# Kernel optimization log

Hardware: AMD Instinct MI355X
Metric: run time of the kernel (lower is better)

Reference implementation:

```python
import jax, jax.numpy as jnp
import numpy as np

E, D, H = 8, 512, 2048  # num_experts, features, features*mlp_ratio
B, S = 4, 512


def _lecun(key, shape):
    fan_in = shape[-2] if len(shape) >= 2 else shape[0]
    return jax.random.normal(key, shape, dtype=jnp.float32) / jnp.sqrt(jnp.float32(fan_in))


def setup_inputs() -> dict:
    key = jax.random.key(0)
    ks = jax.random.split(key, 8)
    return {
        'x_real': jax.random.normal(ks[0], (B, S, D), dtype=jnp.float32),
        'x_imag': jax.random.normal(ks[1], (B, S, D), dtype=jnp.float32),
        # gating Dense over concat([amp, phase]) -> in_features = 2*D
        'gate_W': _lecun(ks[2], (2 * D, E)),
        'gate_b': jnp.zeros((E,), jnp.float32),
        # per-expert ComplexLinear 1: D -> H
        'W1r': _lecun(ks[3], (E, D, H)),
        'W1i': _lecun(ks[4], (E, D, H)),
        'b1r': jnp.zeros((E, H), jnp.float32),
        'b1i': jnp.zeros((E, H), jnp.float32),
        # per-expert ComplexModReLU bias
        'mod_b': jnp.zeros((E, H), jnp.float32),
        # per-expert ComplexLinear 2: H -> D
        'W2r': _lecun(ks[5], (E, H, D)),
        'W2i': _lecun(ks[6], (E, H, D)),
        'b2r': jnp.zeros((E, D), jnp.float32),
        'b2i': jnp.zeros((E, D), jnp.float32),
    }


def reference(x_real, x_imag, gate_W, gate_b, W1r, W1i, b1r, b1i, mod_b, W2r, W2i, b2r, b2i):
    eps = 1e-10
    # --- gating: scores over [|z|, angle(z)] ---
    amp = jnp.sqrt(x_real ** 2 + x_imag ** 2)            # |z|, [B,S,D]
    phase = jnp.arctan2(x_imag, x_real)                  # angle(z)
    routing_input = jnp.concatenate([amp, phase], axis=-1)  # [B,S,2D]
    scores = routing_input @ gate_W + gate_b             # [B,S,E]
    probs = jax.nn.softmax(scores, axis=-1)
    idx = jnp.argmax(probs, axis=-1)                     # [B,S] top-1 expert

    # --- all experts dense (faithful to reference): complex linear 1 ---
    # (Wr + iWi)(xr + ixi) : hr = xr Wr - xi Wi ; hi = xr Wi + xi Wr
    h_r = (jnp.einsum('bsd,edh->ebsh', x_real, W1r)
           - jnp.einsum('bsd,edh->ebsh', x_imag, W1i)) + b1r[:, None, None, :]
    h_i = (jnp.einsum('bsd,edh->ebsh', x_real, W1i)
           + jnp.einsum('bsd,edh->ebsh', x_imag, W1r)) + b1i[:, None, None, :]

    # --- ComplexModReLU: relu(|z|+b) * z / (|z|+eps), |z| = sqrt(r^2+i^2+eps) ---
    a = jnp.sqrt(h_r ** 2 + h_i ** 2 + eps)              # [E,B,S,H]
    scale = jax.nn.relu(a + mod_b[:, None, None, :]) / (a + eps)
    h_r = h_r * scale
    h_i = h_i * scale

    # --- complex linear 2 ---
    o_r = (jnp.einsum('ebsh,ehd->ebsd', h_r, W2r)
           - jnp.einsum('ebsh,ehd->ebsd', h_i, W2i)) + b2r[:, None, None, :]
    o_i = (jnp.einsum('ebsh,ehd->ebsd', h_r, W2i)
           + jnp.einsum('ebsh,ehd->ebsd', h_i, W2r)) + b2i[:, None, None, :]

    # --- mask + weight (top-1): out = sum_e out_e * probs[...,e] * (argmax==e) ---
    e_ids = jnp.arange(probs.shape[-1])
    w = jnp.transpose(probs, (2, 0, 1)) * (idx[None, :, :] == e_ids[:, None, None])  # [E,B,S]
    out_r = jnp.einsum('ebs,ebsd->bsd', w, o_r)
    out_i = jnp.einsum('ebs,ebsd->bsd', w, o_i)
    return (out_r, out_i)
```

## Files before the change

kernel.cpp:

```cpp
#include <hip/hip_runtime.h>
#include <math.h>

#define NE 8
#define ND 512
#define NH 2048
#define NT 2048

typedef __attribute__((ext_vector_type(8))) short short8;
typedef __attribute__((ext_vector_type(4))) float f32x4;

#define GLL(g, d) __builtin_amdgcn_global_load_lds( \
    (const __attribute__((address_space(1))) void*)(g), \
    (__attribute__((address_space(3))) void*)(d), 16, 0, 0)

__device__ __forceinline__ unsigned short f2bf(float x) {
    unsigned int u = __builtin_bit_cast(unsigned int, x);
    u += 0x7FFFu + ((u >> 16) & 1u);
    return (unsigned short)(u >> 16);
}

__device__ __forceinline__ short8 neg8(short8 v) {
    int4 u = __builtin_bit_cast(int4, v);
    u.x ^= 0x80008000; u.y ^= 0x80008000; u.z ^= 0x80008000; u.w ^= 0x80008000;
    return __builtin_bit_cast(short8, u);
}

__device__ __forceinline__ short8 lds8(const unsigned short* p) {
    return *(const short8*)p;
}

__global__ __launch_bounds__(256) void gate_kernel(
    const float* __restrict__ xr, const float* __restrict__ xi,
    const float* __restrict__ gW, const float* __restrict__ gb,
    float* __restrict__ gate_w,
    int* __restrict__ counts, int* __restrict__ tok_list)
{
    int t = blockIdx.x;
    int tid = threadIdx.x;
    const float* xrt = xr + (size_t)t * ND;
    const float* xit = xi + (size_t)t * ND;

    float acc[NE] = {0,0,0,0,0,0,0,0};
    for (int r = tid; r < 2 * ND; r += 256) {
        int d = r & (ND - 1);
        float a = xrt[d], b = xit[d];
        float v = (r < ND) ? sqrtf(a * a + b * b) : atan2f(b, a);
        const float4* g = (const float4*)(gW + (size_t)r * NE);
        float4 g0 = g[0], g1 = g[1];
        acc[0] += v * g0.x; acc[1] += v * g0.y; acc[2] += v * g0.z; acc[3] += v * g0.w;
        acc[4] += v * g1.x; acc[5] += v * g1.y; acc[6] += v * g1.z; acc[7] += v * g1.w;
    }
    #pragma unroll
    for (int e = 0; e < NE; e++) {
        for (int off = 32; off > 0; off >>= 1)
            acc[e] += __shfl_down(acc[e], off, 64);
    }
    __shared__ float part[4][NE];
    int wave = tid >> 6, lane = tid & 63;
    if (lane == 0) {
        #pragma unroll
        for (int e = 0; e < NE; e++) part[wave][e] = acc[e];
    }
    __syncthreads();
    if (tid == 0) {
        float s[NE];
        #pragma unroll
        for (int e = 0; e < NE; e++)
            s[e] = part[0][e] + part[1][e] + part[2][e] + part[3][e] + gb[e];
        int amax = 0; float m = s[0];
        #pragma unroll
        for (int e = 1; e < NE; e++) if (s[e] > m) { m = s[e]; amax = e; }
        float denom = 0.f;
        #pragma unroll
        for (int e = 0; e < NE; e++) denom += expf(s[e] - m);
        gate_w[t] = 1.0f / denom;
        int pos = atomicAdd(&counts[amax], 1);
        tok_list[amax * NT + pos] = t;
    }
}

__global__ __launch_bounds__(256) void convx_kernel(
    const float* __restrict__ xr, const float* __restrict__ xi,
    unsigned short* __restrict__ obr, unsigned short* __restrict__ obi)
{
    int i = blockIdx.x * 256 + threadIdx.x;
    float4 vr = ((const float4*)xr)[i];
    float4 vi = ((const float4*)xi)[i];
    ((ushort4*)obr)[i] = make_ushort4(f2bf(vr.x), f2bf(vr.y), f2bf(vr.z), f2bf(vr.w));
    ((ushort4*)obi)[i] = make_ushort4(f2bf(vi.x), f2bf(vi.y), f2bf(vi.z), f2bf(vi.w));
}

__global__ __launch_bounds__(256) void transw_kernel(
    const float* __restrict__ s0, unsigned short* __restrict__ d0,
    const float* __restrict__ s1, unsigned short* __restrict__ d1,
    int R, int C)
{
    __shared__ float tile[64][65];
    int e = blockIdx.z;
    int c0 = blockIdx.x * 64, r0 = blockIdx.y * 64;
    size_t off = (size_t)e * R * C;
    int tid = threadIdx.x;
    #pragma unroll
    for (int p = 0; p < 2; ++p) {
        const float* src = (p ? s1 : s0) + off;
        unsigned short* dst = (p ? d1 : d0) + off;
        if (p) __syncthreads();
        for (int i = 0; i < 16; ++i) {
            int idx = tid + i * 256;
            int r = idx >> 6, c = idx & 63;
            tile[r][c] = src[(size_t)(r0 + r) * C + c0 + c];
        }
        __syncthreads();
        for (int i = 0; i < 16; ++i) {
            int idx = tid + i * 256;
            int c = idx >> 6, r = idx & 63;
            dst[(size_t)(c0 + c) * R + r0 + r] = f2bf(tile[r][c]);
        }
    }
}

__global__ __launch_bounds__(256, 4) void moe1_kernel(
    const unsigned short* __restrict__ xbr, const unsigned short* __restrict__ xbi,
    const unsigned short* __restrict__ w1tr, const unsigned short* __restrict__ w1ti,
    const float* __restrict__ b1r, const float* __restrict__ b1i,
    const float* __restrict__ mod_b,
    const int* __restrict__ counts, const int* __restrict__ tok_list,
    unsigned short* __restrict__ hr, unsigned short* __restrict__ hi)
{
    int e = blockIdx.z;
    int n = counts[e];
    int mbase = blockIdx.y * 64;
    if (mbase >= n) return;
    int n0 = blockIdx.x * 64;
    int tid = threadIdx.x;
    int w = tid >> 6, l = tid & 63;
    int l15 = l & 15, quad = l >> 4;

    __shared__ unsigned short sAr[64 * 64];
    __shared__ unsigned short sAi[64 * 64];
    __shared__ unsigned short sBr[64 * 64];
    __shared__ unsigned short sBi[64 * 64];
    __shared__ int toks[64];

    const int* tl = tok_list + e * NT;
    if (tid < 64) {
        int idx = mbase + tid;
        toks[tid] = tl[idx < n ? idx : n - 1];
    }
    __syncthreads();

    int swz = (((l & 7) ^ ((l >> 3) & 7)) * 8);
    int ra0 = toks[w * 16 + (l >> 3)];
    int ra1 = toks[w * 16 + 8 + (l >> 3)];
    const unsigned short* gAr0 = xbr + (size_t)ra0 * ND + swz;
    const unsigned short* gAi0 = xbi + (size_t)ra0 * ND + swz;
    const unsigned short* gAr1 = xbr + (size_t)ra1 * ND + swz;
    const unsigned short* gAi1 = xbi + (size_t)ra1 * ND + swz;
    size_t brow = (size_t)e * NH + n0 + w * 16 + (l >> 3);
    const unsigned short* gBr0 = w1tr + brow * ND + swz;
    const unsigned short* gBr1 = w1tr + (brow + 8) * ND + swz;
    const unsigned short* gBi0 = w1ti + brow * ND + swz;
    const unsigned short* gBi1 = w1ti + (brow + 8) * ND + swz;

    unsigned short* dAr0 = sAr + (w * 16) * 64;
    unsigned short* dAr1 = sAr + (w * 16 + 8) * 64;
    unsigned short* dAi0 = sAi + (w * 16) * 64;
    unsigned short* dAi1 = sAi + (w * 16 + 8) * 64;
    unsigned short* dBr0 = sBr + (w * 16) * 64;
    unsigned short* dBr1 = sBr + (w * 16 + 8) * 64;
    unsigned short* dBi0 = sBi + (w * 16) * 64;
    unsigned short* dBi1 = sBi + (w * 16 + 8) * 64;

    f32x4 accr[4] = {}, acci[4] = {};

    for (int kt = 0; kt < ND / 64; ++kt) {
        __syncthreads();
        int ko = kt * 64;
        GLL(gAr0 + ko, dAr0); GLL(gAi0 + ko, dAi0);
        GLL(gAr1 + ko, dAr1); GLL(gAi1 + ko, dAi1);
        GLL(gBr0 + ko, dBr0); GLL(gBr1 + ko, dBr1);
        GLL(gBi0 + ko, dBi0); GLL(gBi1 + ko, dBi1);
        __syncthreads();
        #pragma unroll
        for (int ks = 0; ks < 2; ++ks) {
            int pa = ((ks * 4 + quad) ^ (l15 & 7)) * 8;
            short8 br  = lds8(sBr + (w * 16 + l15) * 64 + pa);
            short8 bi2 = lds8(sBi + (w * 16 + l15) * 64 + pa);
            #pragma unroll
            for (int m = 0; m < 4; ++m) {
                short8 ar  = lds8(sAr + (m * 16 + l15) * 64 + pa);
                short8 ai2 = lds8(sAi + (m * 16 + l15) * 64 + pa);
                short8 an  = neg8(ai2);
                accr[m] = __builtin_amdgcn_mfma_f32_16x16x32_bf16(ar,  br,  accr[m], 0, 0, 0);
                accr[m] = __builtin_amdgcn_mfma_f32_16x16x32_bf16(an,  bi2, accr[m], 0, 0, 0);
                acci[m] = __builtin_amdgcn_mfma_f32_16x16x32_bf16(ar,  bi2, acci[m], 0, 0, 0);
                acci[m] = __builtin_amdgcn_mfma_f32_16x16x32_bf16(ai2, br,  acci[m], 0, 0, 0);
            }
        }
    }

    int col = n0 + w * 16 + l15;
    float bre = b1r[(size_t)e * NH + col];
    float bie = b1i[(size_t)e * NH + col];
    float mbv = mod_b[(size_t)e * NH + col];
    #pragma unroll
    for (int m = 0; m < 4; ++m) {
        #pragma unroll
        for (int r = 0; r < 4; ++r) {
            int tix = m * 16 + quad * 4 + r;
            if (mbase + tix >= n) continue;
            int tok = toks[tix];
            float vr = accr[m][r] + bre;
            float vi = acci[m][r] + bie;
            float a = sqrtf(vr * vr + vi * vi + 1e-10f);
            float sc = fmaxf(a + mbv, 0.0f) / (a + 1e-10f);
            hr[(size_t)tok * NH + col] = f2bf(vr * sc);
            hi[(size_t)tok * NH + col] = f2bf(vi * sc);
        }
    }
}

__global__ __launch_bounds__(256, 4) void moe2_kernel(
    const unsigned short* __restrict__ hr, const unsigned short* __restrict__ hi,
    const unsigned short* __restrict__ w2tr, const unsigned short* __restrict__ w2ti,
    const float* __restrict__ b2r, const float* __restrict__ b2i,
    const int* __restrict__ counts, const int* __restrict__ tok_list,
    const float* __restrict__ gate_w,
    float* __restrict__ out)
{
    int e = blockIdx.z >> 2;
    int ksl = blockIdx.z & 3;
    int n = counts[e];
    int mbase = blockIdx.y * 64;
    if (mbase >= n) return;
    int n0 = blockIdx.x * 64;
    int kbase = ksl * (NH / 4);
    int tid = threadIdx.x;
    int w = tid >> 6, l = tid & 63;
    int l15 = l & 15, quad = l >> 4;

    __shared__ unsigned short sAr[64 * 64];
    __shared__ unsigned short sAi[64 * 64];
    __shared__ unsigned short sBr[64 * 64];
    __shared__ unsigned short sBi[64 * 64];
    __shared__ int toks[64];

    const int* tl = tok_list + e * NT;
    if (tid < 64) {
        int idx = mbase + tid;
        toks[tid] = tl[idx < n ? idx : n - 1];
    }
    __syncthreads();

    int swz = (((l & 7) ^ ((l >> 3) & 7)) * 8);
    int ra0 = toks[w * 16 + (l >> 3)];
    int ra1 = toks[w * 16 + 8 + (l >> 3)];
    const unsigned short* gAr0 = hr + (size_t)ra0 * NH + kbase + swz;
    const unsigned short* gAi0 = hi + (size_t)ra0 * NH + kbase + swz;
    const unsigned short* gAr1 = hr + (size_t)ra1 * NH + kbase + swz;
    const unsigned short* gAi1 = hi + (size_t)ra1 * NH + kbase + swz;
    size_t brow = (size_t)e * ND + n0 + w * 16 + (l >> 3);
    const unsigned short* gBr0 = w2tr + brow * NH + kbase + swz;
    const unsigned short* gBr1 = w2tr + (brow + 8) * NH + kbase + swz;
    const unsigned short* gBi0 = w2ti + brow * NH + kbase + swz;
    const unsigned short* gBi1 = w2ti + (brow + 8) * NH + kbase + swz;

    unsigned short* dAr0 = sAr + (w * 16) * 64;
    unsigned short* dAr1 = sAr + (w * 16 + 8) * 64;
    unsigned short* dAi0 = sAi + (w * 16) * 64;
    unsigned short* dAi1 = sAi + (w * 16 + 8) * 64;
    unsigned short* dBr0 = sBr + (w * 16) * 64;
    unsigned short* dBr1 = sBr + (w * 16 + 8) * 64;
    unsigned short* dBi0 = sBi + (w * 16) * 64;
    unsigned short* dBi1 = sBi + (w * 16 + 8) * 64;

    f32x4 accr[4] = {}, acci[4] = {};

    for (int kt = 0; kt < (NH / 4) / 64; ++kt) {
        __syncthreads();
        int ko = kt * 64;
        GLL(gAr0 + ko, dAr0); GLL(gAi0 + ko, dAi0);
        GLL(gAr1 + ko, dAr1); GLL(gAi1 + ko, dAi1);
        GLL(gBr0 + ko, dBr0); GLL(gBr1 + ko, dBr1);
        GLL(gBi0 + ko, dBi0); GLL(gBi1 + ko, dBi1);
        __syncthreads();
        #pragma unroll
        for (int ks = 0; ks < 2; ++ks) {
            int pa = ((ks * 4 + quad) ^ (l15 & 7)) * 8;
            short8 br  = lds8(sBr + (w * 16 + l15) * 64 + pa);
            short8 bi2 = lds8(sBi + (w * 16 + l15) * 64 + pa);
            #pragma unroll
            for (int m = 0; m < 4; ++m) {
                short8 ar  = lds8(sAr + (m * 16 + l15) * 64 + pa);
                short8 ai2 = lds8(sAi + (m * 16 + l15) * 64 + pa);
                short8 an  = neg8(ai2);
                accr[m] = __builtin_amdgcn_mfma_f32_16x16x32_bf16(ar,  br,  accr[m], 0, 0, 0);
                accr[m] = __builtin_amdgcn_mfma_f32_16x16x32_bf16(an,  bi2, accr[m], 0, 0, 0);
                acci[m] = __builtin_amdgcn_mfma_f32_16x16x32_bf16(ar,  bi2, acci[m], 0, 0, 0);
                acci[m] = __builtin_amdgcn_mfma_f32_16x16x32_bf16(ai2, br,  acci[m], 0, 0, 0);
            }
        }
    }

    int col = n0 + w * 16 + l15;
    float bre = (ksl == 0) ? b2r[(size_t)e * ND + col] : 0.0f;
    float bie = (ksl == 0) ? b2i[(size_t)e * ND + col] : 0.0f;
    #pragma unroll
    for (int m = 0; m < 4; ++m) {
        #pragma unroll
        for (int r = 0; r < 4; ++r) {
            int tix = m * 16 + quad * 4 + r;
            if (mbase + tix >= n) continue;
            int tok = toks[tix];
            float gw = gate_w[tok];
            atomicAdd(&out[(size_t)tok * ND + col], (accr[m][r] + bre) * gw);
            atomicAdd(&out[(size_t)NT * ND + (size_t)tok * ND + col], (acci[m][r] + bie) * gw);
        }
    }
}

extern "C" void kernel_launch(void* const* d_in, const int* in_sizes, int n_in,
                              void* d_out, int out_size, void* d_ws, size_t ws_size,
                              hipStream_t stream) {
    const float* xr   = (const float*)d_in[0];
    const float* xi   = (const float*)d_in[1];
    const float* gW   = (const float*)d_in[2];
    const float* gb   = (const float*)d_in[3];
    const float* W1r  = (const float*)d_in[4];
    const float* W1i  = (const float*)d_in[5];
    const float* b1r  = (const float*)d_in[6];
    const float* b1i  = (const float*)d_in[7];
    const float* modb = (const float*)d_in[8];
    const float* W2r  = (const float*)d_in[9];
    const float* W2i  = (const float*)d_in[10];
    const float* b2r  = (const float*)d_in[11];
    const float* b2i  = (const float*)d_in[12];
    float* out = (float*)d_out;

    char* ws = (char*)d_ws;
    int*   counts   = (int*)ws;
    float* gate_w   = (float*)(ws + 256);
    int*   tok_list = (int*)(ws + 256 + 8192);
    size_t off = 256 + 8192 + (size_t)NE * NT * 4;
    unsigned short* xbr  = (unsigned short*)(ws + off); off += (size_t)NT * ND * 2;
    unsigned short* xbi  = (unsigned short*)(ws + off); off += (size_t)NT * ND * 2;
    unsigned short* w1tr = (unsigned short*)(ws + off); off += (size_t)NE * ND * NH * 2;
    unsigned short* w1ti = (unsigned short*)(ws + off); off += (size_t)NE * ND * NH * 2;
    unsigned short* w2tr = (unsigned short*)(ws + off); off += (size_t)NE * ND * NH * 2;
    unsigned short* w2ti = (unsigned short*)(ws + off); off += (size_t)NE * ND * NH * 2;
    unsigned short* h_r  = (unsigned short*)(ws + off); off += (size_t)NT * NH * 2;
    unsigned short* h_i  = (unsigned short*)(ws + off); off += (size_t)NT * NH * 2;

    hipMemsetAsync(counts, 0, 64 * sizeof(int), stream);
    hipMemsetAsync(out, 0, (size_t)out_size * sizeof(float), stream);
    gate_kernel<<<NT, 256, 0, stream>>>(xr, xi, gW, gb, gate_w, counts, tok_list);
    convx_kernel<<<(NT * ND / 4) / 256, 256, 0, stream>>>(xr, xi, xbr, xbi);
    transw_kernel<<<dim3(NH / 64, ND / 64, NE), 256, 0, stream>>>(W1r, w1tr, W1i, w1ti, ND, NH);
    transw_kernel<<<dim3(ND / 64, NH / 64, NE), 256, 0, stream>>>(W2r, w2tr, W2i, w2ti, NH, ND);
    moe1_kernel<<<dim3(NH / 64, NT / 64, NE), 256, 0, stream>>>(
        xbr, xbi, w1tr, w1ti, b1r, b1i, modb, counts, tok_list, h_r, h_i);
    moe2_kernel<<<dim3(ND / 64, NT / 64, NE * 4), 256, 0, stream>>>(
        h_r, h_i, w2tr, w2ti, b2r, b2i, counts, tok_list, gate_w, out);
}
```

Baseline: 310.9 us.

## Double-buffer LDS in MoE GEMMs, halve moe2 split-K, vectorize weight transpose stores

Both expert GEMM kernels now use two LDS buffers, so the next K tile is loaded through global_load_lds while the current one is computed, with one barrier per step instead of two. The per-block token LDS array is dropped and token ids are read from global memory directly. moe2 goes from a 4-way to a 2-way K split, which halves the atomic adds to the output but launches fewer blocks. The weight transpose now writes 4 bf16 values per store, and LDS use doubles, so launch_bounds drops to 2 blocks per SM.

```diff
diff --git a/kernel.cpp b/kernel.cpp
--- a/kernel.cpp
+++ b/kernel.cpp
@@ -111,15 +111,61 @@
             tile[r][c] = src[(size_t)(r0 + r) * C + c0 + c];
         }
         __syncthreads();
-        for (int i = 0; i < 16; ++i) {
-            int idx = tid + i * 256;
-            int c = idx >> 6, r = idx & 63;
-            dst[(size_t)(c0 + c) * R + r0 + r] = f2bf(tile[r][c]);
+        #pragma unroll
+        for (int i = 0; i < 4; ++i) {
+            int c = i * 16 + (tid >> 4);
+            int r4 = (tid & 15) * 4;
+            ushort4 v = make_ushort4(f2bf(tile[r4][c]), f2bf(tile[r4 + 1][c]),
+                                     f2bf(tile[r4 + 2][c]), f2bf(tile[r4 + 3][c]));
+            *(ushort4*)&dst[(size_t)(c0 + c) * R + r0 + r4] = v;
         }
     }
 }
 
-__global__ __launch_bounds__(256, 4) void moe1_kernel(
+
+#define STAGE_(SA_R, SA_I, SB_R, SB_I, ko) do {  \
+    GLL(gAr0 + (ko), SA_R + (w * 16) * 64);      \
+    GLL(gAi0 + (ko), SA_I + (w * 16) * 64);      \
+    GLL(gAr1 + (ko), SA_R + (w * 16 + 8) * 64);  \
+    GLL(gAi1 + (ko), SA_I + (w * 16 + 8) * 64);  \
+    GLL(gBr0 + (ko), SB_R + (w * 16) * 64);      \
+    GLL(gBr1 + (ko), SB_R + (w * 16 + 8) * 64);  \
+    GLL(gBi0 + (ko), SB_I + (w * 16) * 64);      \
+    GLL(gBi1 + (ko), SB_I + (w * 16 + 8) * 64);  \
+} while (0)
+
+#define COMPUTE_(SA_R, SA_I, SB_R, SB_I) do {                                          \
+    _Pragma("unroll")                                                                  \
+    for (int ks = 0; ks < 2; ++ks) {                                                   \
+        int pa = ((ks * 4 + quad) ^ (l15 & 7)) * 8;                                    \
+        short8 br  = lds8(SB_R + (w * 16 + l15) * 64 + pa);                            \
+        short8 bi2 = lds8(SB_I + (w * 16 + l15) * 64 + pa);                            \
+        _Pragma("unroll")                                                              \
+        for (int m = 0; m < 4; ++m) {                                                  \
+            short8 ar  = lds8(SA_R + (m * 16 + l15) * 64 + pa);                        \
+            short8 ai2 = lds8(SA_I + (m * 16 + l15) * 64 + pa);                        \
+            short8 an  = neg8(ai2);                                                    \
+            accr[m] = __builtin_amdgcn_mfma_f32_16x16x32_bf16(ar,  br,  accr[m], 0, 0, 0); \
+            accr[m] = __builtin_amdgcn_mfma_f32_16x16x32_bf16(an,  bi2, accr[m], 0, 0, 0); \
+            acci[m] = __builtin_amdgcn_mfma_f32_16x16x32_bf16(ar,  bi2, acci[m], 0, 0, 0); \
+            acci[m] = __builtin_amdgcn_mfma_f32_16x16x32_bf16(ai2, br,  acci[m], 0, 0, 0); \
+        }                                                                              \
+    }                                                                                  \
+} while (0)
+
+#define SYNCPIPE do {                                               \
+    asm volatile("s_waitcnt vmcnt(0) lgkmcnt(0)" ::: "memory");     \
+    __builtin_amdgcn_s_barrier();                                   \
+    __builtin_amdgcn_sched_barrier(0);                              \
+} while (0)
+
+#define MOE_LDS_DECL                                                        \
+    __shared__ alignas(16) unsigned short sAr0[4096], sAi0[4096];           \
+    __shared__ alignas(16) unsigned short sBr0[4096], sBi0[4096];           \
+    __shared__ alignas(16) unsigned short sAr1[4096], sAi1[4096];           \
+    __shared__ alignas(16) unsigned short sBr1[4096], sBi1[4096];
+
+__global__ __launch_bounds__(256, 2) void moe1_kernel(
     const unsigned short* __restrict__ xbr, const unsigned short* __restrict__ xbi,
     const unsigned short* __restrict__ w1tr, const unsigned short* __restrict__ w1ti,
     const float* __restrict__ b1r, const float* __restrict__ b1i,
@@ -136,22 +182,14 @@
     int w = tid >> 6, l = tid & 63;
     int l15 = l & 15, quad = l >> 4;
 
-    __shared__ unsigned short sAr[64 * 64];
-    __shared__ unsigned short sAi[64 * 64];
-    __shared__ unsigned short sBr[64 * 64];
-    __shared__ unsigned short sBi[64 * 64];
-    __shared__ int toks[64];
+    MOE_LDS_DECL
 
     const int* tl = tok_list + e * NT;
-    if (tid < 64) {
-        int idx = mbase + tid;
-        toks[tid] = tl[idx < n ? idx : n - 1];
-    }
-    __syncthreads();
-
     int swz = (((l & 7) ^ ((l >> 3) & 7)) * 8);
-    int ra0 = toks[w * 16 + (l >> 3)];
-    int ra1 = toks[w * 16 + 8 + (l >> 3)];
+    int ia0 = mbase + w * 16 + (l >> 3);
+    int ia1 = ia0 + 8;
+    int ra0 = tl[ia0 < n ? ia0 : n - 1];
+    int ra1 = tl[ia1 < n ? ia1 : n - 1];
     const unsigned short* gAr0 = xbr + (size_t)ra0 * ND + swz;
     const unsigned short* gAi0 = xbi + (size_t)ra0 * ND + swz;
     const unsigned short* gAr1 = xbr + (size_t)ra1 * ND + swz;
@@ -162,41 +200,18 @@
     const unsigned short* gBi0 = w1ti + brow * ND + swz;
     const unsigned short* gBi1 = w1ti + (brow + 8) * ND + swz;
 
-    unsigned short* dAr0 = sAr + (w * 16) * 64;
-    unsigned short* dAr1 = sAr + (w * 16 + 8) * 64;
-    unsigned short* dAi0 = sAi + (w * 16) * 64;
-    unsigned short* dAi1 = sAi + (w * 16 + 8) * 64;
-    unsigned short* dBr0 = sBr + (w * 16) * 64;
-    unsigned short* dBr1 = sBr + (w * 16 + 8) * 64;
-    unsigned short* dBi0 = sBi + (w * 16) * 64;
-    unsigned short* dBi1 = sBi + (w * 16 + 8) * 64;
-
     f32x4 accr[4] = {}, acci[4] = {};
 
-    for (int kt = 0; kt < ND / 64; ++kt) {
-        __syncthreads();
-        int ko = kt * 64;
-        GLL(gAr0 + ko, dAr0); GLL(gAi0 + ko, dAi0);
-        GLL(gAr1 + ko, dAr1); GLL(gAi1 + ko, dAi1);
-        GLL(gBr0 + ko, dBr0); GLL(gBr1 + ko, dBr1);
-        GLL(gBi0 + ko, dBi0); GLL(gBi1 + ko, dBi1);
-        __syncthreads();
-        #pragma unroll
-        for (int ks = 0; ks < 2; ++ks) {
-            int pa = ((ks * 4 + quad) ^ (l15 & 7)) * 8;
-            short8 br  = lds8(sBr + (w * 16 + l15) * 64 + pa);
-            short8 bi2 = lds8(sBi + (w * 16 + l15) * 64 + pa);
-            #pragma unroll
-            for (int m = 0; m < 4; ++m) {
-                short8 ar  = lds8(sAr + (m * 16 + l15) * 64 + pa);
-                short8 ai2 = lds8(sAi + (m * 16 + l15) * 64 + pa);
-                short8 an  = neg8(ai2);
-                accr[m] = __builtin_amdgcn_mfma_f32_16x16x32_bf16(ar,  br,  accr[m], 0, 0, 0);
-                accr[m] = __builtin_amdgcn_mfma_f32_16x16x32_bf16(an,  bi2, accr[m], 0, 0, 0);
-                acci[m] = __builtin_amdgcn_mfma_f32_16x16x32_bf16(ar,  bi2, acci[m], 0, 0, 0);
-                acci[m] = __builtin_amdgcn_mfma_f32_16x16x32_bf16(ai2, br,  acci[m], 0, 0, 0);
-            }
-        }
+    STAGE_(sAr0, sAi0, sBr0, sBi0, 0);
+    SYNCPIPE;
+    #pragma unroll 1
+    for (int kt = 0; kt < ND / 64; kt += 2) {
+        if (kt + 1 < ND / 64) STAGE_(sAr1, sAi1, sBr1, sBi1, (kt + 1) * 64);
+        COMPUTE_(sAr0, sAi0, sBr0, sBi0);
+        SYNCPIPE;
+        if (kt + 2 < ND / 64) STAGE_(sAr0, sAi0, sBr0, sBi0, (kt + 2) * 64);
+        COMPUTE_(sAr1, sAi1, sBr1, sBi1);
+        SYNCPIPE;
     }
 
     int col = n0 + w * 16 + l15;
@@ -209,7 +224,7 @@
         for (int r = 0; r < 4; ++r) {
             int tix = m * 16 + quad * 4 + r;
             if (mbase + tix >= n) continue;
-            int tok = toks[tix];
+            int tok = tl[mbase + tix];
             float vr = accr[m][r] + bre;
             float vi = acci[m][r] + bie;
             float a = sqrtf(vr * vr + vi * vi + 1e-10f);
@@ -220,7 +235,7 @@
     }
 }
 
-__global__ __launch_bounds__(256, 4) void moe2_kernel(
+__global__ __launch_bounds__(256, 2) void moe2_kernel(
     const unsigned short* __restrict__ hr, const unsigned short* __restrict__ hi,
     const unsigned short* __restrict__ w2tr, const unsigned short* __restrict__ w2ti,
     const float* __restrict__ b2r, const float* __restrict__ b2i,
@@ -228,33 +243,25 @@
     const float* __restrict__ gate_w,
     float* __restrict__ out)
 {
-    int e = blockIdx.z >> 2;
-    int ksl = blockIdx.z & 3;
+    int e = blockIdx.z >> 1;
+    int ksl = blockIdx.z & 1;
     int n = counts[e];
     int mbase = blockIdx.y * 64;
     if (mbase >= n) return;
     int n0 = blockIdx.x * 64;
-    int kbase = ksl * (NH / 4);
+    int kbase = ksl * (NH / 2);
     int tid = threadIdx.x;
     int w = tid >> 6, l = tid & 63;
     int l15 = l & 15, quad = l >> 4;
 
-    __shared__ unsigned short sAr[64 * 64];
-    __shared__ unsigned short sAi[64 * 64];
-    __shared__ unsigned short sBr[64 * 64];
-    __shared__ unsigned short sBi[64 * 64];
-    __shared__ int toks[64];
+    MOE_LDS_DECL
 
     const int* tl = tok_list + e * NT;
-    if (tid < 64) {
-        int idx = mbase + tid;
-        toks[tid] = tl[idx < n ? idx : n - 1];
-    }
-    __syncthreads();
-
     int swz = (((l & 7) ^ ((l >> 3) & 7)) * 8);
-    int ra0 = toks[w * 16 + (l >> 3)];
-    int ra1 = toks[w * 16 + 8 + (l >> 3)];
+    int ia0 = mbase + w * 16 + (l >> 3);
+    int ia1 = ia0 + 8;
+    int ra0 = tl[ia0 < n ? ia0 : n - 1];
+    int ra1 = tl[ia1 < n ? ia1 : n - 1];
     const unsigned short* gAr0 = hr + (size_t)ra0 * NH + kbase + swz;
     const unsigned short* gAi0 = hi + (size_t)ra0 * NH + kbase + swz;
     const unsigned short* gAr1 = hr + (size_t)ra1 * NH + kbase + swz;
@@ -265,41 +272,18 @@
     const unsigned short* gBi0 = w2ti + brow * NH + kbase + swz;
     const unsigned short* gBi1 = w2ti + (brow + 8) * NH + kbase + swz;
 
-    unsigned short* dAr0 = sAr + (w * 16) * 64;
-    unsigned short* dAr1 = sAr + (w * 16 + 8) * 64;
-    unsigned short* dAi0 = sAi + (w * 16) * 64;
-    unsigned short* dAi1 = sAi + (w * 16 + 8) * 64;
-    unsigned short* dBr0 = sBr + (w * 16) * 64;
-    unsigned short* dBr1 = sBr + (w * 16 + 8) * 64;
-    unsigned short* dBi0 = sBi + (w * 16) * 64;
-    unsigned short* dBi1 = sBi + (w * 16 + 8) * 64;
-
     f32x4 accr[4] = {}, acci[4] = {};
 
-    for (int kt = 0; kt < (NH / 4) / 64; ++kt) {
-        __syncthreads();
-        int ko = kt * 64;
-        GLL(gAr0 + ko, dAr0); GLL(gAi0 + ko, dAi0);
-        GLL(gAr1 + ko, dAr1); GLL(gAi1 + ko, dAi1);
-        GLL(gBr0 + ko, dBr0); GLL(gBr1 + ko, dBr1);
-        GLL(gBi0 + ko, dBi0); GLL(gBi1 + ko, dBi1);
-        __syncthreads();
-        #pragma unroll
-        for (int ks = 0; ks < 2; ++ks) {
-            int pa = ((ks * 4 + quad) ^ (l15 & 7)) * 8;
-            short8 br  = lds8(sBr + (w * 16 + l15) * 64 + pa);
-            short8 bi2 = lds8(sBi + (w * 16 + l15) * 64 + pa);
-            #pragma unroll
-            for (int m = 0; m < 4; ++m) {
-                short8 ar  = lds8(sAr + (m * 16 + l15) * 64 + pa);
-                short8 ai2 = lds8(sAi + (m * 16 + l15) * 64 + pa);
-                short8 an  = neg8(ai2);
-                accr[m] = __builtin_amdgcn_mfma_f32_16x16x32_bf16(ar,  br,  accr[m], 0, 0, 0);
-                accr[m] = __builtin_amdgcn_mfma_f32_16x16x32_bf16(an,  bi2, accr[m], 0, 0, 0);
-                acci[m] = __builtin_amdgcn_mfma_f32_16x16x32_bf16(ar,  bi2, acci[m], 0, 0, 0);
-                acci[m] = __builtin_amdgcn_mfma_f32_16x16x32_bf16(ai2, br,  acci[m], 0, 0, 0);
-            }
-        }
+    STAGE_(sAr0, sAi0, sBr0, sBi0, 0);
+    SYNCPIPE;
+    #pragma unroll 1
+    for (int kt = 0; kt < (NH / 2) / 64; kt += 2) {
+        if (kt + 1 < (NH / 2) / 64) STAGE_(sAr1, sAi1, sBr1, sBi1, (kt + 1) * 64);
+        COMPUTE_(sAr0, sAi0, sBr0, sBi0);
+        SYNCPIPE;
+        if (kt + 2 < (NH / 2) / 64) STAGE_(sAr0, sAi0, sBr0, sBi0, (kt + 2) * 64);
+        COMPUTE_(sAr1, sAi1, sBr1, sBi1);
+        SYNCPIPE;
     }
 
     int col = n0 + w * 16 + l15;
@@ -311,7 +295,7 @@
         for (int r = 0; r < 4; ++r) {
             int tix = m * 16 + quad * 4 + r;
             if (mbase + tix >= n) continue;
-            int tok = toks[tix];
+            int tok = tl[mbase + tix];
             float gw = gate_w[tok];
             atomicAdd(&out[(size_t)tok * ND + col], (accr[m][r] + bre) * gw);
             atomicAdd(&out[(size_t)NT * ND + (size_t)tok * ND + col], (acci[m][r] + bie) * gw);
@@ -359,6 +343,6 @@
     transw_kernel<<<dim3(ND / 64, NH / 64, NE), 256, 0, stream>>>(W2r, w2tr, W2i, w2ti, NH, ND);
     moe1_kernel<<<dim3(NH / 64, NT / 64, NE), 256, 0, stream>>>(
         xbr, xbi, w1tr, w1ti, b1r, b1i, modb, counts, tok_list, h_r, h_i);
-    moe2_kernel<<<dim3(ND / 64, NT / 64, NE * 4), 256, 0, stream>>>(
+    moe2_kernel<<<dim3(ND / 64, NT / 64, NE * 2), 256, 0, stream>>>(
         h_r, h_i, w2tr, w2ti, b2r, b2i, counts, tok_list, gate_w, out);
 }
```

New measurement: 323.4 us. +4.0%, slower.
